# Performance work log

Measured on AMD Instinct MI355X. Metric: run time of the kernel, lower is better.

## Reference

```python
import jax, jax.numpy as jnp
import numpy as np

B, C, T = 8, 256, 4096
IC = C // 2  # inter_channels
BN_EPS = 1e-5


def setup_inputs() -> dict:
    key = jax.random.key(0)
    ks = jax.random.split(key, 12)
    s_in = 1.0 / np.sqrt(C)
    s_ic = 1.0 / np.sqrt(IC)
    return {
        "x": jax.random.normal(ks[0], (B, C, T), dtype=jnp.float32),
        "theta_w": jax.random.uniform(ks[1], (IC, C), jnp.float32, -s_in, s_in),
        "theta_b": jax.random.uniform(ks[2], (IC,), jnp.float32, -s_in, s_in),
        "phi_w": jax.random.uniform(ks[3], (IC, C), jnp.float32, -s_in, s_in),
        "phi_b": jax.random.uniform(ks[4], (IC,), jnp.float32, -s_in, s_in),
        "g_w": jax.random.uniform(ks[5], (IC, C), jnp.float32, -s_in, s_in),
        "g_b": jax.random.uniform(ks[6], (IC,), jnp.float32, -s_in, s_in),
        "w_w": jax.random.uniform(ks[7], (C, IC), jnp.float32, -s_ic, s_ic),
        "w_b": jax.random.uniform(ks[8], (C,), jnp.float32, -s_ic, s_ic),
        "bn_gamma": jax.random.normal(ks[9], (C,), dtype=jnp.float32),
        "bn_beta": jax.random.normal(ks[10], (C,), dtype=jnp.float32),
    }


def _conv1x1(w, b, inp):
    # Conv1d kernel_size=1 == per-position channel matmul
    return jnp.einsum('oc,bct->bot', w, inp) + b[None, :, None]


def _maxpool2(z):
    b, c, t = z.shape
    return z.reshape(b, c, t // 2, 2).max(axis=-1)


def reference(x, theta_w, theta_b, phi_w, phi_b, g_w, g_b, w_w, w_b, bn_gamma, bn_beta):
    theta_x = _conv1x1(theta_w, theta_b, x)              # (B, IC, T)
    phi_x = _maxpool2(_conv1x1(phi_w, phi_b, x))         # (B, IC, T/2)
    g_x = _maxpool2(_conv1x1(g_w, g_b, x))               # (B, IC, T/2)

    # f = theta^T @ phi ; softmax-free, divided by N = T/2
    f = jnp.einsum('bct,bcs->bts', theta_x, phi_x)       # (B, T, T/2)
    f_div_C = f / f.shape[-1]
    y = jnp.einsum('bts,bcs->bct', f_div_C, g_x)         # (B, IC, T)

    w_y = _conv1x1(w_w, w_b, y)                          # (B, C, T)
    # BatchNorm1d (training-mode batch statistics over batch+time)
    mean = w_y.mean(axis=(0, 2), keepdims=True)
    var = w_y.var(axis=(0, 2), keepdims=True)
    w_y = (w_y - mean) * jax.lax.rsqrt(var + BN_EPS)
    w_y = w_y * bn_gamma[None, :, None] + bn_beta[None, :, None]
    return w_y + x
```

## Files before the change

kernel.cpp:

```cpp
#include <hip/hip_runtime.h>
#include <hip/hip_bf16.h>

typedef __attribute__((ext_vector_type(8))) short short8;
typedef __attribute__((ext_vector_type(4))) short short4v;
typedef __attribute__((ext_vector_type(4))) float floatx4;
typedef unsigned int u32;

#define BB 8
#define CC 256
#define ICH 128
#define TT 4096
#define SS 2048
static constexpr float BN_EPS = 1e-5f;
static constexpr float INV_S  = 1.0f / 2048.0f;
static constexpr float INV_BT = 1.0f / 32768.0f;

typedef const __attribute__((address_space(1))) u32* gas_ptr;
typedef __attribute__((address_space(3))) u32* las_ptr;
__device__ __forceinline__ void gl_lds16(const void* g, void* l) {
    __builtin_amdgcn_global_load_lds((gas_ptr)g, (las_ptr)l, 16, 0, 0);
}


__global__ __launch_bounds__(256) void k0x_transpose(
    const float* __restrict__ x, __hip_bfloat16* __restrict__ xt,
    const float* __restrict__ phi_w, const float* __restrict__ g_w,
    __hip_bfloat16* __restrict__ Wf)
{
    const int id = blockIdx.x;
    if (id >= 2048) {
        int idx = (id - 2048) * 256 + threadIdx.x;
        const float* src = (idx < 8192) ? (phi_w + (size_t)idx * 4)
                                        : (g_w + (size_t)(idx - 8192) * 4);
        float4 v = *(const float4*)src;
        alignas(8) __hip_bfloat16 t[4];
        t[0] = __float2bfloat16(v.x); t[1] = __float2bfloat16(v.y);
        t[2] = __float2bfloat16(v.z); t[3] = __float2bfloat16(v.w);
        *(short4v*)(Wf + (size_t)idx * 4) = *(const short4v*)t;
        return;
    }

    __shared__ float Tl[64][65];
    const int b = id & 7, rest = id >> 3;
    const int cb = (rest & 3) * 64, tb = (rest >> 2) * 64;
    const int tid = threadIdx.x;
    #pragma unroll
    for (int it = 0; it < 4; ++it) {
        int idx = tid + 256 * it;
        int row = idx >> 4, c4 = idx & 15;
        float4 v = *(const float4*)(x + ((size_t)b * CC + cb + row) * TT + tb + c4 * 4);
        Tl[row][c4 * 4 + 0] = v.x; Tl[row][c4 * 4 + 1] = v.y;
        Tl[row][c4 * 4 + 2] = v.z; Tl[row][c4 * 4 + 3] = v.w;
    }
    __syncthreads();
    #pragma unroll
    for (int it = 0; it < 2; ++it) {
        int idx = tid + 256 * it;
        int trow = idx >> 3, ch = idx & 7;
        alignas(16) __hip_bfloat16 tmp[8];
        #pragma unroll
        for (int e = 0; e < 8; ++e) tmp[e] = __float2bfloat16(Tl[ch * 8 + e][trow]);
        *(short8*)(xt + ((size_t)b * TT + tb + trow) * CC + cb + ch * 8) = *(const short8*)tmp;
    }
}

__global__ __launch_bounds__(256) void k1_mfma(
    const __hip_bfloat16* __restrict__ Wf, const float* __restrict__ phi_b,
    const float* __restrict__ g_b, const __hip_bfloat16* __restrict__ xt,
    __hip_bfloat16* __restrict__ phi_g)
{
    __shared__ short lds[128 * 132];
    short* As = lds;
    short* Bs = lds + 128 * 64;

    const int id = blockIdx.x;
    const int b  = id & 7;
    const int m0 = ((id >> 3) & 1) * 128;
    const int tb = (id >> 4) * 128;
    const int s0 = (id >> 4) * 64;
    const int tid = threadIdx.x;
    const int w = tid >> 6, l = tid & 63;
    const int quad = l >> 4, lm = l & 15;
    const int wm = (w & 1) * 64, wn = (w >> 1) * 64;
    const int rs = l >> 3, cs = (l & 7) * 8;

    const __hip_bfloat16* Ap = Wf + (size_t)m0 * CC;
    const __hip_bfloat16* Bp = xt + ((size_t)b * TT + tb) * CC;

    floatx4 acc[4][4];
    #pragma unroll
    for (int i = 0; i < 4; ++i)
        #pragma unroll
        for (int j = 0; j < 4; ++j) acc[i][j] = (floatx4)0.f;

    for (int kc = 0; kc < 4; ++kc) {
        const int k0 = kc * 64;
        const int rbase = w * 32;
        #pragma unroll
        for (int t = 0; t < 4; ++t) {
            gl_lds16(Ap + (size_t)(rbase + t * 8 + rs) * CC + k0 + cs, &As[(rbase + t * 8) * 64]);
            gl_lds16(Bp + (size_t)(rbase + t * 8 + rs) * CC + k0 + cs, &Bs[(rbase + t * 8) * 64]);
        }
        __syncthreads();
        #pragma unroll
        for (int ks = 0; ks < 2; ++ks) {
            short8 a[4], bb[4];
            #pragma unroll
            for (int i = 0; i < 4; ++i)
                a[i] = *(const short8*)&As[(wm + i * 16 + lm) * 64 + ks * 32 + quad * 8];
            #pragma unroll
            for (int j = 0; j < 4; ++j)
                bb[j] = *(const short8*)&Bs[(wn + j * 16 + lm) * 64 + ks * 32 + quad * 8];
            #pragma unroll
            for (int i = 0; i < 4; ++i)
                #pragma unroll
                for (int j = 0; j < 4; ++j)
                    acc[i][j] = __builtin_amdgcn_mfma_f32_16x16x32_bf16(a[i], bb[j], acc[i][j], 0, 0, 0);
        }
        __syncthreads();
    }

    __hip_bfloat16* Out = (__hip_bfloat16*)lds;
    #pragma unroll
    for (int i = 0; i < 4; ++i)
        #pragma unroll
        for (int j = 0; j < 4; ++j)
            #pragma unroll
            for (int r = 0; r < 4; ++r)
                Out[(wm + i * 16 + quad * 4 + r) * 132 + wn + j * 16 + lm] =
                    __float2bfloat16(acc[i][j][r]);
    __syncthreads();
    #pragma unroll
    for (int it = 0; it < 4; ++it) {
        int idx = tid + 256 * it;
        int orow = idx >> 3, grp = idx & 7;
        int o = m0 + orow;
        float bias = (o < ICH) ? phi_b[o] : g_b[o - ICH];
        short8 v0 = *(const short8*)&Out[orow * 132 + grp * 16];
        short8 v1 = *(const short8*)&Out[orow * 132 + grp * 16 + 8];
        const __hip_bfloat16* p0 = (const __hip_bfloat16*)&v0;
        const __hip_bfloat16* p1 = (const __hip_bfloat16*)&v1;
        alignas(16) __hip_bfloat16 o8[8];
        #pragma unroll
        for (int e = 0; e < 4; ++e)
            o8[e] = __float2bfloat16(
                fmaxf(__bfloat162float(p0[2 * e]), __bfloat162float(p0[2 * e + 1])) + bias);
        #pragma unroll
        for (int e = 0; e < 4; ++e)
            o8[4 + e] = __float2bfloat16(
                fmaxf(__bfloat162float(p1[2 * e]), __bfloat162float(p1[2 * e + 1])) + bias);
        *(short8*)(phi_g + ((size_t)b * CC + o) * SS + s0 + grp * 8) = *(const short8*)o8;
    }
}

__global__ __launch_bounds__(256) void k2_mfma(
    const __hip_bfloat16* __restrict__ phi_g, float* __restrict__ Mpart)
{
    __shared__ short lds[2 * 128 * 64];
    short* As = lds;
    short* Bs = lds + 128 * 64;
    const int b = blockIdx.x, sc = blockIdx.y;
    const int tid = threadIdx.x;
    const int w = tid >> 6, l = tid & 63;
    const int quad = l >> 4, lm = l & 15;
    const int wm = (w & 1) * 64, wn = (w >> 1) * 64;
    const int rs = l >> 3, cs = (l & 7) * 8;

    const __hip_bfloat16* Ap = phi_g + (size_t)b * CC * SS + sc * 256;
    const __hip_bfloat16* Bp = Ap + (size_t)ICH * SS;

    floatx4 acc[4][4];
    #pragma unroll
    for (int i = 0; i < 4; ++i)
        #pragma unroll
        for (int j = 0; j < 4; ++j) acc[i][j] = (floatx4)0.f;

    for (int kc = 0; kc < 4; ++kc) {
        const int k0 = kc * 64;
        const int rbase = w * 32;
        #pragma unroll
        for (int t = 0; t < 4; ++t) {
            gl_lds16(Ap + (size_t)(rbase + t * 8 + rs) * SS + k0 + cs, &As[(rbase + t * 8) * 64]);
            gl_lds16(Bp + (size_t)(rbase + t * 8 + rs) * SS + k0 + cs, &Bs[(rbase + t * 8) * 64]);
        }
        __syncthreads();
        #pragma unroll
        for (int ks = 0; ks < 2; ++ks) {
            short8 a[4], bb[4];
            #pragma unroll
            for (int i = 0; i < 4; ++i)
                a[i] = *(const short8*)&As[(wm + i * 16 + lm) * 64 + ks * 32 + quad * 8];
            #pragma unroll
            for (int j = 0; j < 4; ++j)
                bb[j] = *(const short8*)&Bs[(wn + j * 16 + lm) * 64 + ks * 32 + quad * 8];
            #pragma unroll
            for (int i = 0; i < 4; ++i)
                #pragma unroll
                for (int j = 0; j < 4; ++j)
                    acc[i][j] = __builtin_amdgcn_mfma_f32_16x16x32_bf16(a[i], bb[j], acc[i][j], 0, 0, 0);
        }
        __syncthreads();
    }

    float* dst = Mpart + ((size_t)(b * 8 + sc)) * ICH * ICH;
    #pragma unroll
    for (int i = 0; i < 4; ++i)
        #pragma unroll
        for (int j = 0; j < 4; ++j)
            #pragma unroll
            for (int r = 0; r < 4; ++r)
                dst[(size_t)(wm + i * 16 + quad * 4 + r) * ICH + wn + j * 16 + lm] = acc[i][j][r];
}

__global__ __launch_bounds__(256) void kpq(
    const float* __restrict__ w_w, const float* __restrict__ Mpart,
    const float* __restrict__ theta_w, const float* __restrict__ theta_b,
    const float* __restrict__ w_b, __hip_bfloat16* __restrict__ P,
    float* __restrict__ q)
{
    __shared__ __align__(16) float ldsf[128 * 68 + 64 * 68];
    const int bid = blockIdx.x;
    const int b    = bid & 7;
    const int rest = bid >> 3;
    const int cob  = (rest >> 2) * 64;
    const int cib  = (rest & 3) * 64;
    const int tid = threadIdx.x;
    const int tx = tid & 15, ty = tid >> 4;

    float accK[2][4][4] = {};
    {
        float (*Al)[65] = (float (*)[65])ldsf;
        float (*Bl)[65] = Al + 64;
        for (int cpb2 = 0; cpb2 < 2; ++cpb2) {
            const int cpb = cpb2 * 64;
            for (int kc2 = 0; kc2 < 2; ++kc2) {
                #pragma unroll
                for (int r = 0; r < 4; ++r) {
                    int idx = tid + 256 * r;
                    int row = idx >> 4, c4 = idx & 15;
                    float4 v = *(const float4*)(w_w + (size_t)(cob + row) * ICH + kc2 * 64 + c4 * 4);
                    Al[c4 * 4 + 0][row] = v.x; Al[c4 * 4 + 1][row] = v.y;
                    Al[c4 * 4 + 2][row] = v.z; Al[c4 * 4 + 3][row] = v.w;
                    float4 s = {0.f, 0.f, 0.f, 0.f};
                    #pragma unroll
                    for (int sc = 0; sc < 8; ++sc) {
                        float4 m = *(const float4*)(Mpart + (((size_t)b * 8 + sc) * ICH + cpb + row) * ICH + kc2 * 64 + c4 * 4);
                        s.x += m.x; s.y += m.y; s.z += m.z; s.w += m.w;
                    }
                    Bl[c4 * 4 + 0][row] = s.x; Bl[c4 * 4 + 1][row] = s.y;
                    Bl[c4 * 4 + 2][row] = s.z; Bl[c4 * 4 + 3][row] = s.w;
                }
                __syncthreads();
                for (int k = 0; k < 64; ++k) {
                    float av[4], bv[4];
                    #pragma unroll
                    for (int i = 0; i < 4; ++i) av[i] = Al[k][ty + 16 * i];
                    #pragma unroll
                    for (int j = 0; j < 4; ++j) bv[j] = Bl[k][tx + 16 * j];
                    #pragma unroll
                    for (int i = 0; i < 4; ++i)
                        #pragma unroll
                        for (int j = 0; j < 4; ++j) accK[cpb2][i][j] += av[i] * bv[j];
                }
                __syncthreads();
            }
        }
    }

    float (*KbL)[68] = (float (*)[68])ldsf;
    #pragma unroll
    for (int cpb2 = 0; cpb2 < 2; ++cpb2)
        #pragma unroll
        for (int i = 0; i < 4; ++i)
            #pragma unroll
            for (int j = 0; j < 4; ++j)
                KbL[cpb2 * 64 + tx + 16 * j][ty + 16 * i] = accK[cpb2][i][j] * INV_S;
    __syncthreads();

    float (*Bt)[68] = (float (*)[68])(ldsf + 128 * 68);
    float acc[4][4] = {};
    for (int kc2 = 0; kc2 < 2; ++kc2) {
        #pragma unroll
        for (int r = 0; r < 4; ++r) {
            int idx = tid + 256 * r;
            int row = idx >> 4, c4 = idx & 15;
            *(float4*)(&Bt[row][c4 * 4]) =
                *(const float4*)(theta_w + (size_t)(kc2 * 64 + row) * CC + cib + c4 * 4);
        }
        __syncthreads();
        for (int k = 0; k < 64; ++k) {
            float av[4], bv[4];
            #pragma unroll
            for (int i = 0; i < 4; ++i) av[i] = KbL[kc2 * 64 + k][ty + 16 * i];
            #pragma unroll
            for (int j = 0; j < 4; ++j) bv[j] = Bt[k][tx + 16 * j];
            #pragma unroll
            for (int i = 0; i < 4; ++i)
                #pragma unroll
                for (int j = 0; j < 4; ++j) acc[i][j] += av[i] * bv[j];
        }
        __syncthreads();
    }
    #pragma unroll
    for (int i = 0; i < 4; ++i)
        #pragma unroll
        for (int j = 0; j < 4; ++j)
            P[((size_t)b * CC + cob + ty + 16 * i) * CC + cib + tx + 16 * j] =
                __float2bfloat16(acc[i][j]);

    if ((rest & 3) == 0 && tid < 64) {
        float s = w_b[cob + tid];
        #pragma unroll 8
        for (int c = 0; c < ICH; ++c) s += KbL[c][tid] * theta_b[c];
        q[b * CC + cob + tid] = s;
    }
}

__global__ __launch_bounds__(256) void k4_mfma(
    const __hip_bfloat16* __restrict__ P, const __hip_bfloat16* __restrict__ xt,
    const float* __restrict__ q, __hip_bfloat16* __restrict__ wy,
    float* __restrict__ pbuf)
{
    __shared__ short lds[128 * 132];
    __shared__ float pst1[4 * 64], pst2[4 * 64];
    short* As = lds;
    short* Bs = lds + 128 * 64;

    const int id = blockIdx.x;
    const int b  = id & 7;
    const int m0 = ((id >> 3) & 1) * 128;
    const int tt = id >> 4;
    const int t0 = tt * 128;
    const int tid = threadIdx.x;
    const int w = tid >> 6, l = tid & 63;
    const int quad = l >> 4, lm = l & 15;
    const int wm = (w & 1) * 64, wn = (w >> 1) * 64;
    const int rs = l >> 3, cs = (l & 7) * 8;

    const __hip_bfloat16* Ap = P + ((size_t)b * CC + m0) * CC;
    const __hip_bfloat16* Bp = xt + ((size_t)b * TT + t0) * CC;

    floatx4 acc[4][4];
    #pragma unroll
    for (int i = 0; i < 4; ++i)
        #pragma unroll
        for (int j = 0; j < 4; ++j) acc[i][j] = (floatx4)0.f;

    for (int kc = 0; kc < 4; ++kc) {
        const int k0 = kc * 64;
        const int rbase = w * 32;
        #pragma unroll
        for (int t = 0; t < 4; ++t) {
            gl_lds16(Ap + (size_t)(rbase + t * 8 + rs) * CC + k0 + cs, &As[(rbase + t * 8) * 64]);
            gl_lds16(Bp + (size_t)(rbase + t * 8 + rs) * CC + k0 + cs, &Bs[(rbase + t * 8) * 64]);
        }
        __syncthreads();
        #pragma unroll
        for (int ks = 0; ks < 2; ++ks) {
            short8 a[4], bb[4];
            #pragma unroll
            for (int i = 0; i < 4; ++i)
                a[i] = *(const short8*)&As[(wm + i * 16 + lm) * 64 + ks * 32 + quad * 8];
            #pragma unroll
            for (int j = 0; j < 4; ++j)
                bb[j] = *(const short8*)&Bs[(wn + j * 16 + lm) * 64 + ks * 32 + quad * 8];
            #pragma unroll
            for (int i = 0; i < 4; ++i)
                #pragma unroll
                for (int j = 0; j < 4; ++j)
                    acc[i][j] = __builtin_amdgcn_mfma_f32_16x16x32_bf16(a[i], bb[j], acc[i][j], 0, 0, 0);
        }
        __syncthreads();
    }

    #pragma unroll
    for (int i = 0; i < 4; ++i) {
        #pragma unroll
        for (int r = 0; r < 4; ++r) {
            int m = wm + i * 16 + quad * 4 + r;
            float bias = q[b * CC + m0 + m];
            float s1 = 0.f, s2 = 0.f;
            #pragma unroll
            for (int j = 0; j < 4; ++j) {
                float v = acc[i][j][r] + bias;
                s1 += v; s2 += v * v;
            }
            #pragma unroll
            for (int off = 1; off < 16; off <<= 1) {
                s1 += __shfl_xor(s1, off);
                s2 += __shfl_xor(s2, off);
            }
            if (lm == 0) {
                pst1[w * 64 + i * 16 + quad * 4 + r] = s1;
                pst2[w * 64 + i * 16 + quad * 4 + r] = s2;
            }
        }
    }

    __hip_bfloat16* Out = (__hip_bfloat16*)lds;
    #pragma unroll
    for (int i = 0; i < 4; ++i) {
        #pragma unroll
        for (int r = 0; r < 4; ++r) {
            int m = wm + i * 16 + quad * 4 + r;
            float bias = q[b * CC + m0 + m];
            #pragma unroll
            for (int j = 0; j < 4; ++j)
                Out[m * 132 + wn + j * 16 + lm] = __float2bfloat16(acc[i][j][r] + bias);
        }
    }
    __syncthreads();

    if (tid < 128) {
        int half = tid >> 6, k = tid & 63;
        float s1 = pst1[half * 64 + k] + pst1[(2 + half) * 64 + k];
        float s2 = pst2[half * 64 + k] + pst2[(2 + half) * 64 + k];
        size_t col = (size_t)b * 32 + tt;
        pbuf[(size_t)(m0 + tid) * 256 + col] = s1;
        pbuf[65536 + (size_t)(m0 + tid) * 256 + col] = s2;
    }

    #pragma unroll
    for (int it = 0; it < 8; ++it) {
        int idx = tid + 256 * it;
        int row = idx >> 4, cg = idx & 15;
        *(short8*)(wy + ((size_t)b * CC + m0 + row) * TT + t0 + cg * 8) =
            *(const short8*)&Out[row * 132 + cg * 8];
    }
}

__global__ __launch_bounds__(256) void k6_out(
    const __hip_bfloat16* __restrict__ wy, const __hip_bfloat16* __restrict__ xt,
    const float* __restrict__ pbuf, const float* __restrict__ gamma,
    const float* __restrict__ beta, float* __restrict__ out)
{
    __shared__ float Fs[64][68];
    __shared__ float cA[64], cB[64];
    const int id = blockIdx.x;
    const int b  = id & 7;
    const int cb = ((id >> 3) & 3) * 64;
    const int tb0 = (id >> 5) * 256;
    const int tid = threadIdx.x;

    {
        const int ch = tid >> 2, qtr = tid & 3;
        const float* p1 = pbuf + (size_t)(cb + ch) * 256 + qtr * 64;
        const float* p2 = p1 + 65536;
        float s1 = 0.f, s2 = 0.f;
        #pragma unroll
        for (int e = 0; e < 16; ++e) {
            float4 a = *(const float4*)(p1 + e * 4);
            float4 c = *(const float4*)(p2 + e * 4);
            s1 += a.x + a.y + a.z + a.w;
            s2 += c.x + c.y + c.z + c.w;
        }
        s1 += __shfl_xor(s1, 1); s1 += __shfl_xor(s1, 2);
        s2 += __shfl_xor(s2, 1); s2 += __shfl_xor(s2, 2);
        if (qtr == 0) {
            float mean = s1 * INV_BT;
            float var  = s2 * INV_BT - mean * mean;
            float A = gamma[cb + ch] * rsqrtf(var + BN_EPS);
            cA[ch] = A;
            cB[ch] = beta[cb + ch] - mean * A;
        }
    }

    for (int tt = 0; tt < 4; ++tt) {
        const int tb = tb0 + tt * 64;
        __syncthreads();
        {
            const int t = tid >> 2, cseg = (tid & 3) * 16;
            const __hip_bfloat16* src = xt + ((size_t)b * TT + tb + t) * CC + cb + cseg;
            short8 v0 = *(const short8*)src;
            short8 v1 = *(const short8*)(src + 8);
            const __hip_bfloat16* p0 = (const __hip_bfloat16*)&v0;
            const __hip_bfloat16* p1 = (const __hip_bfloat16*)&v1;
            #pragma unroll
            for (int e = 0; e < 8; ++e) Fs[t][cseg + e] = __bfloat162float(p0[e]);
            #pragma unroll
            for (int e = 0; e < 8; ++e) Fs[t][cseg + 8 + e] = __bfloat162float(p1[e]);
        }
        __syncthreads();
        {
            const int c = tid >> 2, seg = (tid & 3) * 16;
            const float A = cA[c], Bc = cB[c];
            const __hip_bfloat16* wsrc = wy + ((size_t)b * CC + cb + c) * TT + tb + seg;
            short8 w0 = *(const short8*)wsrc;
            short8 w1 = *(const short8*)(wsrc + 8);
            const __hip_bfloat16* q0 = (const __hip_bfloat16*)&w0;
            const __hip_bfloat16* q1 = (const __hip_bfloat16*)&w1;
            float* dst = out + ((size_t)b * CC + cb + c) * TT + tb + seg;
            #pragma unroll
            for (int e = 0; e < 8; ++e)
                dst[e] = __bfloat162float(q0[e]) * A + Bc + Fs[seg + e][c];
            #pragma unroll
            for (int e = 0; e < 8; ++e)
                dst[8 + e] = __bfloat162float(q1[e]) * A + Bc + Fs[seg + 8 + e][c];
        }
    }
}

extern "C" void kernel_launch(void* const* d_in, const int* in_sizes, int n_in,
                              void* d_out, int out_size, void* d_ws, size_t ws_size,
                              hipStream_t stream)
{
    const float* x        = (const float*)d_in[0];
    const float* theta_w  = (const float*)d_in[1];
    const float* theta_b  = (const float*)d_in[2];
    const float* phi_w    = (const float*)d_in[3];
    const float* phi_b    = (const float*)d_in[4];
    const float* g_w      = (const float*)d_in[5];
    const float* g_b      = (const float*)d_in[6];
    const float* w_w      = (const float*)d_in[7];
    const float* w_b      = (const float*)d_in[8];
    const float* bn_gamma = (const float*)d_in[9];
    const float* bn_beta  = (const float*)d_in[10];
    float* out = (float*)d_out;

    char* p = (char*)d_ws;
    __hip_bfloat16* xt    = (__hip_bfloat16*)p; p += (size_t)8388608 * 2;
    __hip_bfloat16* Wf    = (__hip_bfloat16*)p; p += (size_t)65536 * 2;
    __hip_bfloat16* phi_g = (__hip_bfloat16*)p; p += (size_t)4194304 * 2;
    __hip_bfloat16* P     = (__hip_bfloat16*)p; p += (size_t)524288 * 2;
    float* Mpart = (float*)p; p += (size_t)1048576 * 4;
    float* q     = (float*)p; p += (size_t)2048 * 4;
    __hip_bfloat16* wy = (__hip_bfloat16*)p; p += (size_t)8388608 * 2;
    float* pbuf  = (float*)p;

    k0x_transpose<<<dim3(2112), 256, 0, stream>>>(x, xt, phi_w, g_w, Wf);
    k1_mfma<<<dim3(512), 256, 0, stream>>>(Wf, phi_b, g_b, xt, phi_g);
    k2_mfma<<<dim3(8, 8), 256, 0, stream>>>(phi_g, Mpart);
    kpq<<<dim3(128), 256, 0, stream>>>(w_w, Mpart, theta_w, theta_b, w_b, P, q);
    k4_mfma<<<dim3(512), 256, 0, stream>>>(P, xt, q, wy, pbuf);
    k6_out<<<dim3(512), 256, 0, stream>>>(wy, xt, pbuf, bn_gamma, bn_beta, out);
}
```

Measured before the change: 188.2 us.

## Restructure kpq: reduce Mpart once into LDS, vectorize register-tiled GEMMs

The kpq kernel now sums the eight Mpart slices once into a full 128x128 LDS tile instead of re-reading and re-summing them per chunk. It then runs the w_w x M product with float4 LDS reads and a 4x8 register tile, and reads theta_w directly from global instead of staging it. k2 swaps the A/B operands so it produces the transposed M, and P is written with 4-wide bf16 stores. The goal is fewer redundant global loads and fewer LDS transactions, in exchange for more LDS per block (about 100KB), which may reduce occupancy.

Measured after the change: 183.6 us. -2.5%, faster.

```diff
diff --git a/kernel.cpp b/kernel.cpp
--- a/kernel.cpp
+++ b/kernel.cpp
@@ -166,8 +166,8 @@
     const int wm = (w & 1) * 64, wn = (w >> 1) * 64;
     const int rs = l >> 3, cs = (l & 7) * 8;
 
-    const __hip_bfloat16* Ap = phi_g + (size_t)b * CC * SS + sc * 256;
-    const __hip_bfloat16* Bp = Ap + (size_t)ICH * SS;
+    const __hip_bfloat16* Ap = phi_g + (size_t)b * CC * SS + (size_t)ICH * SS + sc * 256;
+    const __hip_bfloat16* Bp = phi_g + (size_t)b * CC * SS + sc * 256;
 
     floatx4 acc[4][4];
     #pragma unroll
@@ -218,7 +218,8 @@
     const float* __restrict__ w_b, __hip_bfloat16* __restrict__ P,
     float* __restrict__ q)
 {
-    __shared__ __align__(16) float ldsf[128 * 68 + 64 * 68];
+    __shared__ float Ms[128][128];
+    __shared__ float Al[128][68];
     const int bid = blockIdx.x;
     const int b    = bid & 7;
     const int rest = bid >> 3;
@@ -227,86 +228,79 @@
     const int tid = threadIdx.x;
     const int tx = tid & 15, ty = tid >> 4;
 
-    float accK[2][4][4] = {};
     {
-        float (*Al)[65] = (float (*)[65])ldsf;
-        float (*Bl)[65] = Al + 64;
-        for (int cpb2 = 0; cpb2 < 2; ++cpb2) {
-            const int cpb = cpb2 * 64;
-            for (int kc2 = 0; kc2 < 2; ++kc2) {
-                #pragma unroll
-                for (int r = 0; r < 4; ++r) {
-                    int idx = tid + 256 * r;
-                    int row = idx >> 4, c4 = idx & 15;
-                    float4 v = *(const float4*)(w_w + (size_t)(cob + row) * ICH + kc2 * 64 + c4 * 4);
-                    Al[c4 * 4 + 0][row] = v.x; Al[c4 * 4 + 1][row] = v.y;
-                    Al[c4 * 4 + 2][row] = v.z; Al[c4 * 4 + 3][row] = v.w;
-                    float4 s = {0.f, 0.f, 0.f, 0.f};
-                    #pragma unroll
-                    for (int sc = 0; sc < 8; ++sc) {
-                        float4 m = *(const float4*)(Mpart + (((size_t)b * 8 + sc) * ICH + cpb + row) * ICH + kc2 * 64 + c4 * 4);
-                        s.x += m.x; s.y += m.y; s.z += m.z; s.w += m.w;
-                    }
-                    Bl[c4 * 4 + 0][row] = s.x; Bl[c4 * 4 + 1][row] = s.y;
-                    Bl[c4 * 4 + 2][row] = s.z; Bl[c4 * 4 + 3][row] = s.w;
-                }
-                __syncthreads();
-                for (int k = 0; k < 64; ++k) {
-                    float av[4], bv[4];
-                    #pragma unroll
-                    for (int i = 0; i < 4; ++i) av[i] = Al[k][ty + 16 * i];
-                    #pragma unroll
-                    for (int j = 0; j < 4; ++j) bv[j] = Bl[k][tx + 16 * j];
-                    #pragma unroll
-                    for (int i = 0; i < 4; ++i)
-                        #pragma unroll
-                        for (int j = 0; j < 4; ++j) accK[cpb2][i][j] += av[i] * bv[j];
-                }
-                __syncthreads();
+        const float* src = Mpart + (size_t)b * 8 * ICH * ICH;
+        #pragma unroll
+        for (int e = 0; e < 16; ++e) {
+            int f = e * 256 + tid;
+            float4 s = *(const float4*)(src + (size_t)f * 4);
+            #pragma unroll
+            for (int sc = 1; sc < 8; ++sc) {
+                float4 m = *(const float4*)(src + (size_t)sc * ICH * ICH + (size_t)f * 4);
+                s.x += m.x; s.y += m.y; s.z += m.z; s.w += m.w;
             }
-        }
-    }
-
-    float (*KbL)[68] = (float (*)[68])ldsf;
-    #pragma unroll
-    for (int cpb2 = 0; cpb2 < 2; ++cpb2)
+            *(float4*)&Ms[f >> 5][(f & 31) * 4] = s;
+        }
+    }
+    #pragma unroll
+    for (int it = 0; it < 8; ++it) {
+        int idx = tid + 256 * it;
+        int row = idx & 63, c4 = idx >> 6;
+        float4 v = *(const float4*)(w_w + (size_t)(cob + row) * ICH + c4 * 4);
+        Al[c4 * 4 + 0][row] = v.x; Al[c4 * 4 + 1][row] = v.y;
+        Al[c4 * 4 + 2][row] = v.z; Al[c4 * 4 + 3][row] = v.w;
+    }
+    __syncthreads();
+
+    float accK[4][8] = {};
+    #pragma unroll 4
+    for (int k = 0; k < 128; ++k) {
+        float4 av = *(const float4*)&Al[k][ty * 4];
+        float4 b0 = *(const float4*)&Ms[k][tx * 4];
+        float4 b1 = *(const float4*)&Ms[k][64 + tx * 4];
+        const float* avp = (const float*)&av;
+        const float* b0p = (const float*)&b0;
+        const float* b1p = (const float*)&b1;
+        #pragma unroll
+        for (int i = 0; i < 4; ++i) {
+            #pragma unroll
+            for (int j = 0; j < 4; ++j) {
+                accK[i][j]     += avp[i] * b0p[j];
+                accK[i][4 + j] += avp[i] * b1p[j];
+            }
+        }
+    }
+    __syncthreads();
+
+    float (*KbL)[68] = Al;
+    #pragma unroll
+    for (int i = 0; i < 4; ++i)
+        #pragma unroll
+        for (int jj = 0; jj < 8; ++jj)
+            KbL[(jj >> 2) * 64 + tx * 4 + (jj & 3)][ty * 4 + i] = accK[i][jj] * INV_S;
+    __syncthreads();
+
+    float acc[4][4] = {};
+    #pragma unroll 8
+    for (int k = 0; k < 128; ++k) {
+        float4 av = *(const float4*)&KbL[k][ty * 4];
+        float4 bv = *(const float4*)(theta_w + (size_t)k * CC + cib + tx * 4);
+        const float* avp = (const float*)&av;
+        const float* bvp = (const float*)&bv;
         #pragma unroll
         for (int i = 0; i < 4; ++i)
             #pragma unroll
             for (int j = 0; j < 4; ++j)
-                KbL[cpb2 * 64 + tx + 16 * j][ty + 16 * i] = accK[cpb2][i][j] * INV_S;
-    __syncthreads();
-
-    float (*Bt)[68] = (float (*)[68])(ldsf + 128 * 68);
-    float acc[4][4] = {};
-    for (int kc2 = 0; kc2 < 2; ++kc2) {
-        #pragma unroll
-        for (int r = 0; r < 4; ++r) {
-            int idx = tid + 256 * r;
-            int row = idx >> 4, c4 = idx & 15;
-            *(float4*)(&Bt[row][c4 * 4]) =
-                *(const float4*)(theta_w + (size_t)(kc2 * 64 + row) * CC + cib + c4 * 4);
-        }
-        __syncthreads();
-        for (int k = 0; k < 64; ++k) {
-            float av[4], bv[4];
-            #pragma unroll
-            for (int i = 0; i < 4; ++i) av[i] = KbL[kc2 * 64 + k][ty + 16 * i];
-            #pragma unroll
-            for (int j = 0; j < 4; ++j) bv[j] = Bt[k][tx + 16 * j];
-            #pragma unroll
-            for (int i = 0; i < 4; ++i)
-                #pragma unroll
-                for (int j = 0; j < 4; ++j) acc[i][j] += av[i] * bv[j];
-        }
-        __syncthreads();
-    }
-    #pragma unroll
-    for (int i = 0; i < 4; ++i)
-        #pragma unroll
-        for (int j = 0; j < 4; ++j)
-            P[((size_t)b * CC + cob + ty + 16 * i) * CC + cib + tx + 16 * j] =
-                __float2bfloat16(acc[i][j]);
+                acc[i][j] += avp[i] * bvp[j];
+    }
+    #pragma unroll
+    for (int i = 0; i < 4; ++i) {
+        alignas(8) __hip_bfloat16 o4[4];
+        #pragma unroll
+        for (int j = 0; j < 4; ++j) o4[j] = __float2bfloat16(acc[i][j]);
+        *(short4v*)(P + ((size_t)b * CC + cob + ty * 4 + i) * CC + cib + tx * 4) =
+            *(const short4v*)o4;
+    }
 
     if ((rest & 3) == 0 && tid < 64) {
         float s = w_b[cob + tid];
```
